# Performance work log

Hardware: AMD Instinct MI355X
Metric: run time of the kernel (lower is better)

## Reference

```python
import jax, jax.numpy as jnp
import numpy as np

N_HEADS = 16
ROPE_BASE = 10000.0

def rotate_half(x):
    x1, x2 = jnp.split(x, 2, axis=-1)
    return jnp.concatenate([-x2, x1], axis=-1)

def rope_tables(T, D, dtype):
    inv_freq = 1.0 / (ROPE_BASE ** (np.arange(0, D, 2, dtype=np.float32) / D))
    t = np.arange(T, dtype=np.float32)
    freqs = np.outer(t, inv_freq)            # [T, D/2]
    emb = np.concatenate([freqs, freqs], -1)  # [T, D]
    return jnp.asarray(np.cos(emb), dtype), jnp.asarray(np.sin(emb), dtype)

def setup_inputs() -> dict:
    key = jax.random.key(0)
    ks = jax.random.split(key, 5)
    B, T, C, D = 2, 2048, 1024, 64
    s = 0.02
    return {
        "x":  jax.random.normal(ks[0], (B, T, C), jnp.float32),
        "Wq": jax.random.normal(ks[1], (C, C), jnp.float32) * s,
        "Wk": jax.random.normal(ks[2], (C, D), jnp.float32) * s,
        "Wv": jax.random.normal(ks[3], (C, D), jnp.float32) * s,
        "Wo": jax.random.normal(ks[4], (C, C), jnp.float32) * s,
    }

def reference(x, Wq, Wk, Wv, Wo):
    B, T, C = x.shape
    H = N_HEADS
    D = C // H
    scale = D ** -0.5
    q = (x @ Wq).reshape(B, T, H, D).transpose(0, 2, 1, 3)  # [B,H,T,D]
    k = x @ Wk                                              # [B,T,D] single KV head
    v = x @ Wv                                              # [B,T,D]
    cos, sin = rope_tables(T, D, x.dtype)                   # [T,D]
    q = q * cos + rotate_half(q) * sin                      # broadcast over B,H
    k = k * cos + rotate_half(k) * sin                      # broadcast over B
    # MQA causal attention: shared K/V head broadcast to all query heads
    scores = jnp.einsum('bhqd,bkd->bhqk', q, k) * scale     # [B,H,T,T]
    causal = jnp.tril(jnp.ones((T, T), bool))
    scores = jnp.where(causal, scores, jnp.finfo(scores.dtype).min)
    attn = jax.nn.softmax(scores, axis=-1)
    out = jnp.einsum('bhqk,bkd->bhqd', attn, v)             # [B,H,T,D]
    out = out.transpose(0, 2, 1, 3).reshape(B, T, C)
    return out @ Wo
```

## Files before the change

### kernel.cpp

```cpp
#include <hip/hip_runtime.h>
#include <hip/hip_bf16.h>

typedef _Float16 f16;
typedef __attribute__((ext_vector_type(8))) _Float16 f16x8;
typedef __attribute__((ext_vector_type(4))) _Float16 f16x4;
typedef __attribute__((ext_vector_type(4))) float f32x4;

#define MFMA16(a, b, c) __builtin_amdgcn_mfma_f32_16x16x32_f16(a, b, c, 0, 0, 0)

__device__ __forceinline__ void gload_lds16(const void* g, void* l)
{
    __builtin_amdgcn_global_load_lds(
        (const __attribute__((address_space(1))) unsigned int*)g,
        (__attribute__((address_space(3))) unsigned int*)l, 16, 0, 0);
}

__global__ __launch_bounds__(256) void cvt_all_kernel(const float* __restrict__ x, const float* __restrict__ Wq,
                                                      const float* __restrict__ Wk, const float* __restrict__ Wv,
                                                      const float* __restrict__ Wo, f16* __restrict__ xb,
                                                      f16* __restrict__ WallT, f16* __restrict__ WoT)
{
    int i = blockIdx.x * 256 + threadIdx.x;
    if (i < 1048576) {
        float4 v = ((const float4*)x)[i];
        f16x4 o;
        o[0] = (f16)v.x; o[1] = (f16)v.y; o[2] = (f16)v.z; o[3] = (f16)v.w;
        *(f16x4*)(xb + 4 * (size_t)i) = o;
        return;
    }
    const float* src;
    f16* dstbase;
    int n4, k4, ldN;
    if (i < 1114112) {
        int j = i - 1048576;
        n4 = (j & 255) * 4; k4 = (j >> 8) * 4;
        src = Wq; ldN = 1024; dstbase = WallT + (size_t)n4 * 1024;
    } else if (i < 1122304) {
        int j = i - 1114112;
        int p4 = (j & 31) * 4; k4 = (j >> 5) * 4;
        if (p4 < 64) {
            n4 = (p4 >= 16 && p4 < 48) ? (p4 ^ 48) : p4;
            src = Wk;
        } else {
            n4 = p4 - 64;
            src = Wv;
        }
        ldN = 64; dstbase = WallT + (size_t)(1024 + p4) * 1024;
    } else {
        int j = i - 1122304;
        n4 = (j & 255) * 4; k4 = (j >> 8) * 4;
        src = Wo; ldN = 1024; dstbase = WoT + (size_t)n4 * 1024;
    }
    float4 v0 = *(const float4*)(src + (size_t)(k4 + 0) * ldN + n4);
    float4 v1 = *(const float4*)(src + (size_t)(k4 + 1) * ldN + n4);
    float4 v2 = *(const float4*)(src + (size_t)(k4 + 2) * ldN + n4);
    float4 v3 = *(const float4*)(src + (size_t)(k4 + 3) * ldN + n4);
    float a0[4] = {v0.x, v0.y, v0.z, v0.w};
    float a1[4] = {v1.x, v1.y, v1.z, v1.w};
    float a2[4] = {v2.x, v2.y, v2.z, v2.w};
    float a3[4] = {v3.x, v3.y, v3.z, v3.w};
#pragma unroll
    for (int jj = 0; jj < 4; ++jj) {
        f16x4 o;
        o[0] = (f16)a0[jj]; o[1] = (f16)a1[jj]; o[2] = (f16)a2[jj]; o[3] = (f16)a3[jj];
        *(f16x4*)(dstbase + (size_t)jj * 1024 + k4) = o;
    }
}

template<int MODE>
__global__ __launch_bounds__(256) void gemm_bt(const f16* __restrict__ A, const f16* __restrict__ Bt,
                                               void* __restrict__ Cv, f16* __restrict__ kout, f16* __restrict__ vout,
                                               int NBX)
{
    __shared__ __align__(16) f16 As[128 * 64];
    __shared__ __align__(16) f16 Bs[64 * 64];
    int id = blockIdx.x;
    int qn = gridDim.x >> 3;
    int lin = (id & 7) * qn + (id >> 3);
    int bx = lin % NBX, by = lin / NBX;
    int tid = threadIdx.x, lane = tid & 63, wid = tid >> 6;
    int wr = wid >> 1, wc = wid & 1;
    int lrow = lane & 15, gq = lane >> 4;
    f32x4 acc[4][2];
#pragma unroll
    for (int fm = 0; fm < 4; ++fm)
#pragma unroll
        for (int fn = 0; fn < 2; ++fn) acc[fm][fn] = (f32x4){0.f, 0.f, 0.f, 0.f};

    for (int kt = 0; kt < 16; ++kt) {
        int k0 = kt * 64;
#pragma unroll
        for (int i = 0; i < 4; ++i) {
            int c = wid * 4 + i;
            int row = c * 8 + (lane >> 3);
            int slot = (lane & 7) ^ (row & 7);
            gload_lds16(A + (size_t)(by * 128 + row) * 1024 + k0 + slot * 8, &As[c * 512 + lane * 8]);
        }
#pragma unroll
        for (int i = 0; i < 2; ++i) {
            int c = wid * 2 + i;
            int row = c * 8 + (lane >> 3);
            int slot = (lane & 7) ^ (row & 7);
            gload_lds16(Bt + (size_t)(bx * 64 + row) * 1024 + k0 + slot * 8, &Bs[c * 512 + lane * 8]);
        }
        __syncthreads();
#pragma unroll
        for (int ks = 0; ks < 2; ++ks) {
            f16x8 af[4], bf[2];
#pragma unroll
            for (int fm = 0; fm < 4; ++fm) {
                int row = wr * 64 + fm * 16 + lrow;
                int slot = (ks * 4 + gq) ^ (row & 7);
                af[fm] = *(const f16x8*)&As[row * 64 + slot * 8];
            }
#pragma unroll
            for (int fn = 0; fn < 2; ++fn) {
                int row = wc * 32 + fn * 16 + lrow;
                int slot = (ks * 4 + gq) ^ (row & 7);
                bf[fn] = *(const f16x8*)&Bs[row * 64 + slot * 8];
            }
#pragma unroll
            for (int fm = 0; fm < 4; ++fm)
#pragma unroll
                for (int fn = 0; fn < 2; ++fn)
                    acc[fm][fn] = MFMA16(af[fm], bf[fn], acc[fm][fn]);
        }
        __syncthreads();
    }
    if constexpr (MODE == 1) {
        float* C = (float*)Cv;
#pragma unroll
        for (int fm = 0; fm < 4; ++fm)
#pragma unroll
            for (int fn = 0; fn < 2; ++fn)
#pragma unroll
                for (int r = 0; r < 4; ++r) {
                    int row = by * 128 + wr * 64 + fm * 16 + gq * 4 + r;
                    int col = bx * 64 + wc * 32 + fn * 16 + lrow;
                    C[(size_t)row * 1024 + col] = acc[fm][fn][r];
                }
    } else {
        if (bx < 16) {
            f16* C = (f16*)Cv;
#pragma unroll
            for (int fm = 0; fm < 4; ++fm)
#pragma unroll
                for (int fn = 0; fn < 2; ++fn)
#pragma unroll
                    for (int r = 0; r < 4; ++r) {
                        int row = by * 128 + wr * 64 + fm * 16 + gq * 4 + r;
                        int col = bx * 64 + wc * 32 + fn * 16 + lrow;
                        C[(size_t)row * 1024 + col] = (f16)acc[fm][fn][r];
                    }
        } else if (bx == 16) {
            const float L2B = 13.287712379549449f / 64.0f;
            int i = wc * 16 + lrow;
            float invf = exp2f(-(float)(2 * i) * L2B);
#pragma unroll
            for (int fm = 0; fm < 4; ++fm)
#pragma unroll
                for (int r = 0; r < 4; ++r) {
                    int row = by * 128 + wr * 64 + fm * 16 + gq * 4 + r;
                    float t = (float)(row & 2047);
                    float ss, cc;
                    sincosf(t * invf, &ss, &cc);
                    float x1 = acc[fm][0][r], x2 = acc[fm][1][r];
                    kout[(size_t)row * 64 + i]      = (f16)(x1 * cc - x2 * ss);
                    kout[(size_t)row * 64 + i + 32] = (f16)(x2 * cc + x1 * ss);
                }
        } else {
#pragma unroll
            for (int fm = 0; fm < 4; ++fm)
#pragma unroll
                for (int fn = 0; fn < 2; ++fn) {
                    int d = wc * 32 + fn * 16 + lrow;
                    int rowbase = by * 128 + wr * 64 + fm * 16 + gq * 4;
                    f16x4 pw;
#pragma unroll
                    for (int r = 0; r < 4; ++r) pw[r] = (f16)acc[fm][fn][r];
                    *(f16x4*)&vout[(size_t)d * 4096 + rowbase] = pw;
                }
        }
    }
}

#define SOFTMAX(S, MM, LL, OO, PSF) do {                                            \
    float mx = fmaxf(fmaxf(fmaxf(S[0][0],S[0][1]),fmaxf(S[0][2],S[0][3])),          \
                     fmaxf(fmaxf(S[1][0],S[1][1]),fmaxf(S[1][2],S[1][3])));         \
    mx = fmaxf(mx, fmaxf(fmaxf(fmaxf(S[2][0],S[2][1]),fmaxf(S[2][2],S[2][3])),      \
                         fmaxf(fmaxf(S[3][0],S[3][1]),fmaxf(S[3][2],S[3][3]))));    \
    mx = fmaxf(mx, __shfl_xor(mx, 16));                                             \
    mx = fmaxf(mx, __shfl_xor(mx, 32));                                             \
    if (!__all(mx <= MM + 3.0f)) {                                                  \
        float mn = fmaxf(MM, mx);                                                   \
        float alpha = exp2f(MM - mn);                                               \
        MM = mn; LL *= alpha;                                                       \
        float av0 = __shfl(alpha, g * 4 + 0), av1 = __shfl(alpha, g * 4 + 1);       \
        float av2 = __shfl(alpha, g * 4 + 2), av3 = __shfl(alpha, g * 4 + 3);       \
        _Pragma("unroll")                                                           \
        for (int dt = 0; dt < 4; ++dt) {                                            \
            OO[dt][0] *= av0; OO[dt][1] *= av1; OO[dt][2] *= av2; OO[dt][3] *= av3; \
        }                                                                           \
    }                                                                               \
    float rs = 0.f;                                                                 \
    _Pragma("unroll")                                                               \
    for (int tt = 0; tt < 4; ++tt) {                                                \
        f16x4 pw;                                                                   \
        _Pragma("unroll")                                                           \
        for (int r = 0; r < 4; ++r) {                                               \
            float pp = exp2f(S[tt][r] - MM); S[tt][r] = pp; pw[r] = (f16)pp;        \
        }                                                                           \
        rs += (S[tt][0] + S[tt][1]) + (S[tt][2] + S[tt][3]);                        \
        *(f16x4*)&PSF[lrow * 64 + ((tt * 16 + g * 4) ^ swl)] = pw;                  \
    }                                                                               \
    LL += rs;                                                                       \
} while (0)

__global__ __launch_bounds__(256, 6) void attn_kernel(const f16* __restrict__ q, const f16* __restrict__ k,
                                                      const f16* __restrict__ vt, f16* __restrict__ ao,
                                                      char* __restrict__ partial)
{
    constexpr int T = 2048;
    int c = blockIdx.x, bh = blockIdx.y;
    int b = bh >> 4, h = bh & 15;
    int qt, ch;
    if (c < 16)      { qt = 16 + c; ch = 0; }
    else if (c < 32) { qt = c;      ch = 1; }
    else             { qt = 47 - c; ch = 0; }
    int nt = qt + 1;
    int nch = (qt >= 16) ? 2 : 1;
    int tbeg = ch * 16;
    int tend = min(nt, tbeg + 16);

    int tid = threadIdx.x, lane = tid & 63, wid = tid >> 6;
    int lrow = lane & 15, g = lane >> 4;
    int qw = qt * 64 + wid * 16;
    int swl = (lrow & 7) << 3;

    __shared__ f16 Ks[64 * 64];
    __shared__ f16 Vs[64 * 64];
    __shared__ f16 PsB[4][16 * 64];

    const f16* qrow = q + (size_t)(b * T + qw + lrow) * 1024 + h * 64;
    f16x8 x0 = *(const f16x8*)&qrow[g * 8];
    f16x8 x1 = *(const f16x8*)&qrow[g * 8 + 32];
    f16x8 qf0, qf1;
    {
        const float qsc = 0.125f * 1.4426950408889634f;
        const float L2B = 13.287712379549449f / 64.0f;
        float t_ = (float)(qw + lrow);
#pragma unroll
        for (int j = 0; j < 8; ++j) {
            int i = g * 8 + j;
            float invf = exp2f(-(float)(2 * i) * L2B);
            float ss, cc;
            sincosf(t_ * invf, &ss, &cc);
            float a0 = (float)x0[j], a1 = (float)x1[j];
            qf0[j] = (f16)((a0 * cc - a1 * ss) * qsc);
            qf1[j] = (f16)((a1 * cc + a0 * ss) * qsc);
        }
    }

    float m = -1e30f, l = 0.f;
    f32x4 o[4];
#pragma unroll
    for (int dt = 0; dt < 4; ++dt) o[dt] = (f32x4){0.f, 0.f, 0.f, 0.f};

    int sr = tid >> 2;
    int sc = (tid & 3) * 16;
    int sw = (sr & 7) << 3;
    const f16* kbase = k + (size_t)b * T * 64;
    const f16* vtbase = vt + (size_t)b * T;

    {
        const f16* kb = kbase + (size_t)(tbeg * 64 + sr) * 64 + sc;
        f16x8 ka = ((const f16x8*)kb)[0], kb2 = ((const f16x8*)kb)[1];
        const f16* vb = vtbase + (size_t)sr * 4096 + tbeg * 64 + sc;
        f16x8 va = ((const f16x8*)vb)[0], vb2 = ((const f16x8*)vb)[1];
        *(f16x8*)&Ks[sr * 64 + (sc ^ sw)]       = ka;
        *(f16x8*)&Ks[sr * 64 + ((sc + 8) ^ sw)] = kb2;
        *(f16x8*)&Vs[sr * 64 + (sc ^ sw)]       = va;
        *(f16x8*)&Vs[sr * 64 + ((sc + 8) ^ sw)] = vb2;
    }
    __syncthreads();

    for (int t = tbeg; t < tend; ++t) {
        bool hasnext = (t + 1 < tend);
        f16x8 kn0, kn1, vn0, vn1;
        if (hasnext) {
            const f16* kb = kbase + (size_t)((t + 1) * 64 + sr) * 64 + sc;
            kn0 = ((const f16x8*)kb)[0];
            kn1 = ((const f16x8*)kb)[1];
            const f16* vb = vtbase + (size_t)sr * 4096 + (t + 1) * 64 + sc;
            vn0 = ((const f16x8*)vb)[0];
            vn1 = ((const f16x8*)vb)[1];
        }
        f16* Ps = &PsB[wid][0];

        f32x4 s[4];
#pragma unroll
        for (int tt = 0; tt < 4; ++tt) {
            f16x8 kf0 = *(const f16x8*)&Ks[(tt * 16 + lrow) * 64 + ((g * 8) ^ swl)];
            f16x8 kf1 = *(const f16x8*)&Ks[(tt * 16 + lrow) * 64 + ((32 + g * 8) ^ swl)];
            f32x4 z = (f32x4){0.f, 0.f, 0.f, 0.f};
            z = MFMA16(kf0, qf0, z);
            z = MFMA16(kf1, qf1, z);
            s[tt] = z;
        }
        if (t == nt - 1) {
            int qab = qw + lrow;
            int kb0 = t * 64 + g * 4;
#pragma unroll
            for (int tt = 0; tt < 4; ++tt)
#pragma unroll
                for (int r = 0; r < 4; ++r)
                    if (kb0 + tt * 16 + r > qab) s[tt][r] = -1e30f;
        }
        SOFTMAX(s, m, l, o, Ps);
#pragma unroll
        for (int chk = 0; chk < 2; ++chk) {
            f16x8 pf = *(const f16x8*)&Ps[lrow * 64 + ((chk * 32 + g * 8) ^ swl)];
#pragma unroll
            for (int dt = 0; dt < 4; ++dt) {
                f16x8 vf = *(const f16x8*)&Vs[(dt * 16 + lrow) * 64 + ((chk * 32 + g * 8) ^ swl)];
                o[dt] = MFMA16(pf, vf, o[dt]);
            }
        }
        if (hasnext) {
            __syncthreads();
            *(f16x8*)&Ks[sr * 64 + (sc ^ sw)]       = kn0;
            *(f16x8*)&Ks[sr * 64 + ((sc + 8) ^ sw)] = kn1;
            *(f16x8*)&Vs[sr * 64 + (sc ^ sw)]       = vn0;
            *(f16x8*)&Vs[sr * 64 + ((sc + 8) ^ sw)] = vn1;
            __syncthreads();
        }
    }
    l += __shfl_xor(l, 16);
    l += __shfl_xor(l, 32);
    float lv[4];
#pragma unroll
    for (int rr = 0; rr < 4; ++rr) lv[rr] = __shfl(l, g * 4 + rr);

    if (nch == 1) {
#pragma unroll
        for (int rr = 0; rr < 4; ++rr) {
            float inv = 1.f / lv[rr];
            int qab = qw + g * 4 + rr;
#pragma unroll
            for (int dt = 0; dt < 4; ++dt)
                ao[(size_t)(b * T + qab) * 1024 + h * 64 + dt * 16 + lrow] = (f16)(o[dt][rr] * inv);
        }
    } else {
        char* slot = partial + ((size_t)(bh * 16 + (qt - 16)) * 2 + ch) * 8704;
        f16* op = (f16*)slot;
        float* mp = (float*)(slot + 8192);
        float* lp = mp + 64;
#pragma unroll
        for (int rr = 0; rr < 4; ++rr) {
            int row = wid * 16 + g * 4 + rr;
#pragma unroll
            for (int dt = 0; dt < 4; ++dt)
                op[row * 64 + dt * 16 + lrow] = (f16)o[dt][rr];
        }
        if (g == 0) { mp[wid * 16 + lrow] = m; lp[wid * 16 + lrow] = l; }
    }
}

__global__ __launch_bounds__(256) void combine_kernel(const char* __restrict__ partial, f16* __restrict__ ao)
{
    constexpr int T = 2048;
    int qt = 16 + blockIdx.x, bh = blockIdx.y;
    int b = bh >> 4, h = bh & 15;
    int tid = threadIdx.x;
    int row = tid >> 2, dp = (tid & 3) * 16;
    const char* s0 = partial + ((size_t)(bh * 16 + (qt - 16)) * 2) * 8704;
    const char* s1 = s0 + 8704;
    const f16* o0 = (const f16*)s0; const float* m0 = (const float*)(s0 + 8192); const float* l0 = m0 + 64;
    const f16* o1 = (const f16*)s1; const float* m1 = (const float*)(s1 + 8192); const float* l1 = m1 + 64;
    float mm0 = m0[row], mm1 = m1[row];
    float M = fmaxf(mm0, mm1);
    float a0 = exp2f(mm0 - M), a1 = exp2f(mm1 - M);
    float inv = 1.f / (l0[row] * a0 + l1[row] * a1);
    f16x8 u0 = ((const f16x8*)(o0 + row * 64 + dp))[0];
    f16x8 u1 = ((const f16x8*)(o0 + row * 64 + dp))[1];
    f16x8 w0 = ((const f16x8*)(o1 + row * 64 + dp))[0];
    f16x8 w1 = ((const f16x8*)(o1 + row * 64 + dp))[1];
    f16x8 r0, r1;
#pragma unroll
    for (int j = 0; j < 8; ++j) {
        r0[j] = (f16)(((float)u0[j] * a0 + (float)w0[j] * a1) * inv);
        r1[j] = (f16)(((float)u1[j] * a0 + (float)w1[j] * a1) * inv);
    }
    f16* dst = ao + (size_t)(b * T + qt * 64 + row) * 1024 + h * 64 + dp;
    *(f16x8*)dst = r0;
    *(f16x8*)(dst + 8) = r1;
}

extern "C" void kernel_launch(void* const* d_in, const int* in_sizes, int n_in,
                              void* d_out, int out_size, void* d_ws, size_t ws_size,
                              hipStream_t stream)
{
    (void)in_sizes; (void)n_in; (void)out_size; (void)ws_size;
    const float* x  = (const float*)d_in[0];
    const float* Wq = (const float*)d_in[1];
    const float* Wk = (const float*)d_in[2];
    const float* Wv = (const float*)d_in[3];
    const float* Wo = (const float*)d_in[4];
    float* out = (float*)d_out;

    char* w = (char*)d_ws;
    size_t off = 0;
    auto alloc = [&](size_t bytes) -> void* {
        void* p = (void*)(w + off);
        off += (bytes + 255) & ~(size_t)255;
        return p;
    };
    f16* xb    = (f16*)alloc(4194304ull * 2);
    f16* WallT = (f16*)alloc(1179648ull * 2);
    f16* WoT   = (f16*)alloc(1048576ull * 2);
    f16* qg    = (f16*)alloc(4194304ull * 2);
    f16* krp   = (f16*)alloc(262144ull * 2);
    f16* vt    = (f16*)alloc(262144ull * 2);
    f16* ao    = (f16*)alloc(4194304ull * 2);
    char* partial = (char*)xb;

    cvt_all_kernel<<<4640, 256, 0, stream>>>(x, Wq, Wk, Wv, Wo, xb, WallT, WoT);
    gemm_bt<0><<<576, 256, 0, stream>>>(xb, WallT, qg, krp, vt, 18);
    attn_kernel<<<dim3(48, 32), 256, 0, stream>>>(qg, krp, vt, ao, partial);
    combine_kernel<<<dim3(16, 32), 256, 0, stream>>>(partial, ao);
    gemm_bt<1><<<512, 256, 0, stream>>>(ao, WoT, out, nullptr, nullptr, 16);
}
```

Measured before the change: 116.1 us.

## Double-buffer K/V tiles in LDS using direct global-to-LDS async loads

Replaces the register-staged K/V prefetch with global_load_lds writes straight into a second LDS buffer, alternating buffers each tile. This cuts the two barriers per iteration to one and removes the register cost of holding the next tile. LDS use doubles for K/V, so the launch-bounds occupancy hint drops from 6 to 4 blocks. Correctness relies on the barrier at the end of each iteration covering completion of the async LDS loads.

```diff
diff --git a/kernel.cpp b/kernel.cpp
--- a/kernel.cpp
+++ b/kernel.cpp
@@ -216,7 +216,7 @@
     LL += rs;                                                                       \
 } while (0)
 
-__global__ __launch_bounds__(256, 6) void attn_kernel(const f16* __restrict__ q, const f16* __restrict__ k,
+__global__ __launch_bounds__(256, 4) void attn_kernel(const f16* __restrict__ q, const f16* __restrict__ k,
                                                       const f16* __restrict__ vt, f16* __restrict__ ao,
                                                       char* __restrict__ partial)
 {
@@ -237,9 +237,9 @@
     int qw = qt * 64 + wid * 16;
     int swl = (lrow & 7) << 3;
 
-    __shared__ f16 Ks[64 * 64];
-    __shared__ f16 Vs[64 * 64];
-    __shared__ f16 PsB[4][16 * 64];
+    __shared__ __align__(16) f16 Ks[2][64 * 64];
+    __shared__ __align__(16) f16 Vs[2][64 * 64];
+    __shared__ __align__(16) f16 PsB[4][16 * 64];
 
     const f16* qrow = q + (size_t)(b * T + qw + lrow) * 1024 + h * 64;
     f16x8 x0 = *(const f16x8*)&qrow[g * 8];
@@ -266,42 +266,38 @@
 #pragma unroll
     for (int dt = 0; dt < 4; ++dt) o[dt] = (f32x4){0.f, 0.f, 0.f, 0.f};
 
-    int sr = tid >> 2;
-    int sc = (tid & 3) * 16;
-    int sw = (sr & 7) << 3;
     const f16* kbase = k + (size_t)b * T * 64;
     const f16* vtbase = vt + (size_t)b * T;
 
-    {
-        const f16* kb = kbase + (size_t)(tbeg * 64 + sr) * 64 + sc;
-        f16x8 ka = ((const f16x8*)kb)[0], kb2 = ((const f16x8*)kb)[1];
-        const f16* vb = vtbase + (size_t)sr * 4096 + tbeg * 64 + sc;
-        f16x8 va = ((const f16x8*)vb)[0], vb2 = ((const f16x8*)vb)[1];
-        *(f16x8*)&Ks[sr * 64 + (sc ^ sw)]       = ka;
-        *(f16x8*)&Ks[sr * 64 + ((sc + 8) ^ sw)] = kb2;
-        *(f16x8*)&Vs[sr * 64 + (sc ^ sw)]       = va;
-        *(f16x8*)&Vs[sr * 64 + ((sc + 8) ^ sw)] = vb2;
-    }
+    int srow_lo = lane >> 3, sslot = lane & 7;
+#define STAGE(buf, t) do {                                                                   \
+    _Pragma("unroll")                                                                        \
+    for (int i_ = 0; i_ < 2; ++i_) {                                                         \
+        int c2 = wid * 2 + i_;                                                               \
+        int row = c2 * 8 + srow_lo;                                                          \
+        int slot = sslot ^ (row & 7);                                                        \
+        gload_lds16(kbase + (size_t)((t) * 64 + row) * 64 + slot * 8,                        \
+                    &Ks[buf][c2 * 512 + lane * 8]);                                          \
+        gload_lds16(vtbase + (size_t)row * 4096 + (t) * 64 + slot * 8,                       \
+                    &Vs[buf][c2 * 512 + lane * 8]);                                          \
+    }                                                                                        \
+} while (0)
+
+    STAGE(0, tbeg);
     __syncthreads();
+    int cur = 0;
 
     for (int t = tbeg; t < tend; ++t) {
-        bool hasnext = (t + 1 < tend);
-        f16x8 kn0, kn1, vn0, vn1;
-        if (hasnext) {
-            const f16* kb = kbase + (size_t)((t + 1) * 64 + sr) * 64 + sc;
-            kn0 = ((const f16x8*)kb)[0];
-            kn1 = ((const f16x8*)kb)[1];
-            const f16* vb = vtbase + (size_t)sr * 4096 + (t + 1) * 64 + sc;
-            vn0 = ((const f16x8*)vb)[0];
-            vn1 = ((const f16x8*)vb)[1];
-        }
+        if (t + 1 < tend) STAGE(cur ^ 1, t + 1);
         f16* Ps = &PsB[wid][0];
+        const f16* Kc = &Ks[cur][0];
+        const f16* Vc = &Vs[cur][0];
 
         f32x4 s[4];
 #pragma unroll
         for (int tt = 0; tt < 4; ++tt) {
-            f16x8 kf0 = *(const f16x8*)&Ks[(tt * 16 + lrow) * 64 + ((g * 8) ^ swl)];
-            f16x8 kf1 = *(const f16x8*)&Ks[(tt * 16 + lrow) * 64 + ((32 + g * 8) ^ swl)];
+            f16x8 kf0 = *(const f16x8*)&Kc[(tt * 16 + lrow) * 64 + ((g * 8) ^ swl)];
+            f16x8 kf1 = *(const f16x8*)&Kc[(tt * 16 + lrow) * 64 + ((32 + g * 8) ^ swl)];
             f32x4 z = (f32x4){0.f, 0.f, 0.f, 0.f};
             z = MFMA16(kf0, qf0, z);
             z = MFMA16(kf1, qf1, z);
@@ -322,19 +318,14 @@
             f16x8 pf = *(const f16x8*)&Ps[lrow * 64 + ((chk * 32 + g * 8) ^ swl)];
 #pragma unroll
             for (int dt = 0; dt < 4; ++dt) {
-                f16x8 vf = *(const f16x8*)&Vs[(dt * 16 + lrow) * 64 + ((chk * 32 + g * 8) ^ swl)];
+                f16x8 vf = *(const f16x8*)&Vc[(dt * 16 + lrow) * 64 + ((chk * 32 + g * 8) ^ swl)];
                 o[dt] = MFMA16(pf, vf, o[dt]);
             }
         }
-        if (hasnext) {
-            __syncthreads();
-            *(f16x8*)&Ks[sr * 64 + (sc ^ sw)]       = kn0;
-            *(f16x8*)&Ks[sr * 64 + ((sc + 8) ^ sw)] = kn1;
-            *(f16x8*)&Vs[sr * 64 + (sc ^ sw)]       = vn0;
-            *(f16x8*)&Vs[sr * 64 + ((sc + 8) ^ sw)] = vn1;
-            __syncthreads();
-        }
-    }
+        __syncthreads();
+        cur ^= 1;
+    }
+#undef STAGE
     l += __shfl_xor(l, 16);
     l += __shfl_xor(l, 32);
     float lv[4];
```

After: 110.0 us. 1.06x faster.
